# Optimization experiments

Hardware: AMD Instinct MI355X
Metric: run time of the kernel (lower is better)

## Reference

```python
import jax, jax.numpy as jnp
import numpy as np

DIM = 2048; N_HEADS = 16; Q_RANK = 1536; KV_RANK = 192
NOPE = 128; ROPE = 64; QK_HD = NOPE + ROPE  # 192 == KV_RANK (required by k_norm/cache widths)
B = 2; S = 2048; MAX_SEQ = 2048
EPS = 1e-6
SCALE = QK_HD ** -0.5


def _rms(v, w):
    return v * jax.lax.rsqrt(jnp.mean(v * v, axis=-1, keepdims=True) + EPS) * w


def _rope(v, cos, sin):
    # v: [..., d] with interleaved (even, odd) pairs, cos/sin broadcastable to [..., d//2]
    vr = v.reshape(v.shape[:-1] + (-1, 2))
    a, b = vr[..., 0], vr[..., 1]
    return jnp.stack([a * cos - b * sin, a * sin + b * cos], axis=-1).reshape(v.shape)


def setup_inputs() -> dict:
    key = jax.random.key(0)
    ks = jax.random.split(key, 8)
    std = 0.02
    x = jax.random.normal(ks[0], (B, S, DIM), jnp.float32)
    # rotary tables: [S, ROPE//2, 2] = (cos, sin)
    t = jnp.arange(S, dtype=jnp.float32)
    inv = 1.0 / (10000.0 ** (jnp.arange(0, ROPE, 2, dtype=jnp.float32) / ROPE))
    ang = jnp.outer(t, inv)
    freqs_cis = jnp.stack([jnp.cos(ang), jnp.sin(ang)], axis=-1)
    mask = jnp.triu(jnp.full((S, S), -1e9, jnp.float32), k=1)  # causal additive mask
    c_kv_cache = jnp.zeros((B, MAX_SEQ, KV_RANK), jnp.float32)
    return {
        "x": x, "start_pos": 0, "freqs_cis": freqs_cis, "mask": mask,
        "c_kv_cache": c_kv_cache,
        "wqa_w": jax.random.normal(ks[1], (Q_RANK, DIM), jnp.float32) * std,
        "wqa_b": jnp.zeros((Q_RANK,), jnp.float32),
        "wqb_w": jax.random.normal(ks[2], (N_HEADS * QK_HD, Q_RANK), jnp.float32) * std,
        "wqb_b": jnp.zeros((N_HEADS * QK_HD,), jnp.float32),
        "q_norm_w": jnp.ones((Q_RANK,), jnp.float32),
        "wkva_w": jax.random.normal(ks[3], (QK_HD, DIM), jnp.float32) * std,
        "wkva_b": jnp.zeros((QK_HD,), jnp.float32),
        "k_norm_w": jnp.ones((KV_RANK,), jnp.float32),
        "wuk_w": jax.random.normal(ks[4], (NOPE, NOPE), jnp.float32) * std,
        "wuk_b": jnp.zeros((NOPE,), jnp.float32),
        "wuv_w": jax.random.normal(ks[5], (DIM, NOPE), jnp.float32) * std,
        "wuv_b": jnp.zeros((DIM,), jnp.float32),
    }


def reference(x, start_pos, freqs_cis, mask, c_kv_cache,
              wqa_w, wqa_b, wqb_w, wqb_b, q_norm_w,
              wkva_w, wkva_b, k_norm_w, wuk_w, wuk_b, wuv_w, wuv_b):
    bsz, seqlen, _ = x.shape
    end = start_pos + seqlen
    cos, sin = freqs_cis[..., 0], freqs_cis[..., 1]  # [seqlen, ROPE//2]

    # low-rank Q path: down-proj -> RMSNorm -> up-proj -> per-head split
    q = _rms(x @ wqa_w.T + wqa_b, q_norm_w)
    q = (q @ wqb_w.T + wqb_b).reshape(bsz, seqlen, N_HEADS, QK_HD)
    q_nope, q_pe = q[..., :NOPE], q[..., NOPE:]
    q_pe = _rope(q_pe, cos[None, :, None, :], sin[None, :, None, :])

    # latent KV path: project -> RMSNorm -> partial RoPE -> scatter into cache
    kv = _rms(x @ wkva_w.T + wkva_b, k_norm_w)  # [b, s, KV_RANK]
    k_pe = _rope(kv[..., NOPE:], cos[None, :, :], sin[None, :, :])
    kv = jnp.concatenate([kv[..., :NOPE], k_pe], axis=-1)
    cache = jax.lax.dynamic_update_slice(c_kv_cache, kv, (0, start_pos, 0))
    keys = cache[:bsz, :end]  # [b, t, KV_RANK]
    k_nope, k_rope = keys[..., :NOPE], keys[..., NOPE:]

    # absorbed attention: fold w_uk into the query side, attend in latent space
    q_abs = q_nope @ wuk_w.T + wuk_b  # [b, s, h, NOPE]
    scores = (jnp.einsum('bshd,btd->bsht', q_abs, k_nope)
              + jnp.einsum('bshr,btr->bsht', q_pe, k_rope)) * SCALE
    scores = scores + mask[None, :seqlen, None, :end]
    attn = jax.nn.softmax(scores, axis=-1)
    out = jnp.einsum('bsht,btd->bshd', attn, k_nope)  # latent values
    out = (out @ wuv_w.T + wuv_b).sum(axis=2)  # up-project values, merge heads -> [b, s, dim]
    return out
```

## Files before the change

kernel.cpp:

```cpp
#include <hip/hip_runtime.h>
#include <hip/hip_bf16.h>
#include <stdint.h>

#define NH     16
#define QRANK  1536
#define NOPE_  128
#define QKHD   192
#define B_     2
#define S_     2048
#define MAXSEQ 2048
#define EPS_   1e-6f
#define SCALE_ 0.07216878364870322f

typedef __attribute__((ext_vector_type(4))) float f32x4;
typedef __attribute__((ext_vector_type(8))) short short8;
typedef __attribute__((ext_vector_type(4))) short short4v;

__device__ inline short f2bf(float f){
  uint32_t u = __builtin_bit_cast(uint32_t, f);
  uint32_t r = (u + 0x7FFFu + ((u >> 16) & 1u)) >> 16;
  return (short)(uint16_t)r;
}
__device__ inline float bf2f(short s){
  uint32_t u = ((uint32_t)(uint16_t)s) << 16;
  return __builtin_bit_cast(float, u);
}

__global__ void k_f2b(const float* __restrict__ in, short* __restrict__ out, long n){
  long i = ((long)blockIdx.x * blockDim.x + threadIdx.x) * 4;
  long stride = (long)gridDim.x * blockDim.x * 4;
  for(; i < n; i += stride){
    float4 v = *reinterpret_cast<const float4*>(in + i);
    short4v o;
    o.x = f2bf(v.x); o.y = f2bf(v.y); o.z = f2bf(v.z); o.w = f2bf(v.w);
    *reinterpret_cast<short4v*>(out + i) = o;
  }
}

template<int BN, bool OUT_BF16>
__global__ __launch_bounds__(256)
void k_gemm_bt(const short* __restrict__ A, const short* __restrict__ Bm,
               const float* __restrict__ bias, float biasScale,
               void* __restrict__ Cp, int M, int N, int K, int ldc)
{
  constexpr int BM = 128, PAD = 40;
  constexpr int WN = BN / 2, FN = WN / 16;
  __shared__ short As[BM * PAD];
  __shared__ short Bs[BN * PAD];
  const int tid = threadIdx.x;
  const int l = tid & 63, wid = tid >> 6;
  const int wr = wid >> 1, wc = wid & 1;
  const long m0 = (long)blockIdx.x * BM;
  const long n0 = (long)blockIdx.y * BN;
  const int lrow = l & 15, lk = (l >> 4) * 8;

  f32x4 acc[4][FN];
  for(int m = 0; m < 4; m++) for(int n = 0; n < FN; n++) acc[m][n] = (f32x4)0.0f;

  for(int kt = 0; kt < K; kt += 32){
    #pragma unroll
    for(int i = 0; i < BM/64; i++){
      int c = tid + 256*i;
      int row = c >> 2, ko = (c & 3) * 8;
      short8 v = *reinterpret_cast<const short8*>(&A[(m0 + row)*(long)K + kt + ko]);
      *reinterpret_cast<short8*>(&As[row*PAD + ko]) = v;
    }
    #pragma unroll
    for(int i = 0; i < BN/64; i++){
      int c = tid + 256*i;
      int row = c >> 2, ko = (c & 3) * 8;
      short8 v = *reinterpret_cast<const short8*>(&Bm[(n0 + row)*(long)K + kt + ko]);
      *reinterpret_cast<short8*>(&Bs[row*PAD + ko]) = v;
    }
    __syncthreads();
    short8 af[4], bfv[FN];
    #pragma unroll
    for(int m = 0; m < 4; m++)
      af[m] = *reinterpret_cast<const short8*>(&As[(wr*64 + m*16 + lrow)*PAD + lk]);
    #pragma unroll
    for(int n = 0; n < FN; n++)
      bfv[n] = *reinterpret_cast<const short8*>(&Bs[(wc*WN + n*16 + lrow)*PAD + lk]);
    #pragma unroll
    for(int m = 0; m < 4; m++)
      #pragma unroll
      for(int n = 0; n < FN; n++)
        acc[m][n] = __builtin_amdgcn_mfma_f32_16x16x32_bf16(af[m], bfv[n], acc[m][n], 0, 0, 0);
    __syncthreads();
  }
  #pragma unroll
  for(int m = 0; m < 4; m++){
    int row_l = wr*64 + m*16 + (l >> 4)*4;
    #pragma unroll
    for(int n = 0; n < FN; n++){
      int col = (int)n0 + wc*WN + n*16 + (l & 15);
      float bv = bias ? bias[col]*biasScale : 0.0f;
      #pragma unroll
      for(int r = 0; r < 4; r++){
        long row = m0 + row_l + r;
        float v = acc[m][n][r] + bv;
        if constexpr (OUT_BF16) ((short*)Cp)[row*(long)ldc + col] = f2bf(v);
        else                    ((float*)Cp)[row*(long)ldc + col] = v;
      }
    }
  }
}

__global__ __launch_bounds__(256)
void k_rms_q(const float* __restrict__ in, const float* __restrict__ w,
             short* __restrict__ out)
{
  const int row = blockIdx.x;
  const int tid = threadIdx.x;
  const float* p = in + (long)row * QRANK;
  float v[6]; float ss = 0.0f;
  #pragma unroll
  for(int i = 0; i < 6; i++){ v[i] = p[tid + 256*i]; ss += v[i]*v[i]; }
  #pragma unroll
  for(int off = 1; off < 64; off <<= 1) ss += __shfl_xor(ss, off);
  __shared__ float red[4];
  if((tid & 63) == 0) red[tid >> 6] = ss;
  __syncthreads();
  ss = red[0] + red[1] + red[2] + red[3];
  float scale = rsqrtf(ss / (float)QRANK + EPS_);
  #pragma unroll
  for(int i = 0; i < 6; i++){
    int c = tid + 256*i;
    out[(long)row*QRANK + c] = f2bf(v[i] * scale * w[c]);
  }
}

__global__ __launch_bounds__(256)
void k_qassemble(const short* __restrict__ q, const float* __restrict__ freqs,
                 short* __restrict__ qn, short* __restrict__ qfull)
{
  int wid = threadIdx.x >> 6, l = threadIdx.x & 63;
  long hr = (long)blockIdx.x*4 + wid;
  long bs = hr >> 4; int h = (int)(hr & 15);
  int s = (int)(bs & (S_ - 1));
  const short* src = q + bs*3072 + h*QKHD;
  qn[hr*128 + l]      = src[l];
  qn[hr*128 + 64 + l] = src[64 + l];
  float v = bf2f(src[128 + l]);
  int i = l >> 1;
  float cs = freqs[(s*32 + i)*2], sn = freqs[(s*32 + i)*2 + 1];
  float pv = __shfl_xor(v, 1);
  float r = (l & 1) ? (pv*sn + v*cs) : (v*cs - pv*sn);
  qfull[hr*QKHD + 128 + l] = f2bf(r);
}

__global__ __launch_bounds__(256)
void k_kvproc(const float* __restrict__ kvf, const float* __restrict__ w,
              const float* __restrict__ freqs, const float* __restrict__ cache,
              const int* __restrict__ sp_ptr, short* __restrict__ kf)
{
  int wid = threadIdx.x >> 6, l = threadIdx.x & 63;
  long row = (long)blockIdx.x*4 + wid;
  int b = (int)(row >> 11);
  int t = (int)(row & (MAXSEQ - 1));
  int sp = sp_ptr[0];
  int end = sp + S_;
  if(t < sp){
    const float* c = cache + row*QKHD;
    kf[row*QKHD + l]       = f2bf(c[l]);
    kf[row*QKHD + 64 + l]  = f2bf(c[64 + l]);
    kf[row*QKHD + 128 + l] = f2bf(c[128 + l]);
    return;
  }
  if(t >= end) return;
  int s = t - sp;
  const float* p = kvf + ((long)b*S_ + s)*QKHD;
  float v0 = p[l], v1 = p[64 + l], v2 = p[128 + l];
  float ss = v0*v0 + v1*v1 + v2*v2;
  #pragma unroll
  for(int off = 1; off < 64; off <<= 1) ss += __shfl_xor(ss, off);
  float scale = rsqrtf(ss / (float)QKHD + EPS_);
  float n0 = v0*scale*w[l], n1 = v1*scale*w[64 + l], n2 = v2*scale*w[128 + l];
  kf[row*QKHD + l]      = f2bf(n0);
  kf[row*QKHD + 64 + l] = f2bf(n1);
  int i = l >> 1;
  float cs = freqs[(s*32 + i)*2], sn = freqs[(s*32 + i)*2 + 1];
  float pv = __shfl_xor(n2, 1);
  float r = (l & 1) ? (pv*sn + n2*cs) : (n2*cs - pv*sn);
  kf[row*QKHD + 128 + l] = f2bf(r);
}

__global__ __launch_bounds__(256)
void k_vtrans(const short* __restrict__ kf, short* __restrict__ vt)
{
  __shared__ short T[32 * 132];
  const int b = blockIdx.y;
  const int t0 = blockIdx.x * 32;
  const int tid = threadIdx.x;
  #pragma unroll
  for(int i = 0; i < 4; i++){
    int c = tid + 256*i;
    int tr = c >> 5, dg = c & 31;
    short4v v = *reinterpret_cast<const short4v*>(&kf[((long)b*MAXSEQ + t0 + tr)*QKHD + dg*4]);
    *reinterpret_cast<short4v*>(&T[tr*132 + dg*4]) = v;
  }
  __syncthreads();
  #pragma unroll
  for(int i = 0; i < 4; i++){
    int c = tid + 256*i;
    int dr = c >> 3, tg = c & 7;
    short4v v;
    v.x = T[(tg*4 + 0)*132 + dr];
    v.y = T[(tg*4 + 1)*132 + dr];
    v.z = T[(tg*4 + 2)*132 + dr];
    v.w = T[(tg*4 + 3)*132 + dr];
    *reinterpret_cast<short4v*>(&vt[((long)b*128 + dr)*MAXSEQ + t0 + tg*4]) = v;
  }
}

__global__ __launch_bounds__(256, 3)
void k_attn3(const short* __restrict__ qfull, const short* __restrict__ kf,
             const short* __restrict__ vt, const int* __restrict__ sp_ptr,
             short* __restrict__ oh)
{
  __shared__ short Ks[64 * 192];
  __shared__ short Vs[128 * 64];
  __shared__ short Ps[4][16 * 68];
  const int tid = threadIdx.x;
  const int l = tid & 63, w = tid >> 6;
  const int lrow = l & 15, lhi = l >> 4;
  const int h = blockIdx.y, b = blockIdx.z;
  const int sp = sp_ptr[0];
  const long kbase = (long)b * MAXSEQ;
  const long vbase = (long)b * 128;

  short8 kreg[6], vreg[4];

  #pragma unroll 1
  for(int part = 0; part < 2; part++){
    const int tile = part ? (31 - (int)blockIdx.x) : (int)blockIdx.x;
    const int q0 = tile * 64;

    short8 qa[6];
    {
      int s = q0 + w*16 + lrow;
      const short* qp = qfull + (((long)b*S_ + s)*NH + h)*QKHD + lhi*8;
      #pragma unroll
      for(int ks = 0; ks < 6; ks++) qa[ks] = *reinterpret_cast<const short8*>(qp + ks*32);
    }
    f32x4 o[8];
    #pragma unroll
    for(int df = 0; df < 8; df++) o[df] = (f32x4)0.0f;
    float mrun[4], lrun[4];
    #pragma unroll
    for(int i = 0; i < 4; i++){ mrun[i] = -1e30f; lrun[i] = 0.0f; }

    int hi = q0 + 64 + sp;
    int nt = (hi + 63) >> 6; if(nt > (MAXSEQ >> 6)) nt = MAXSEQ >> 6;

    {
      const int T0 = 0;
      #pragma unroll
      for(int i = 0; i < 6; i++){
        int cid = tid + 256*i;  int r = cid/24, c = cid%24;
        kreg[i] = *reinterpret_cast<const short8*>(&kf[(kbase + T0 + r)*QKHD + c*8]);
      }
      #pragma unroll
      for(int i = 0; i < 4; i++){
        int cid = tid + 256*i;  int r = cid >> 3, c = cid & 7;
        vreg[i] = *reinterpret_cast<const short8*>(&vt[(vbase + r)*MAXSEQ + T0 + c*8]);
      }
      #pragma unroll
      for(int i = 0; i < 6; i++){
        int cid = tid + 256*i;  int r = cid/24, c = cid%24;
        *reinterpret_cast<short8*>(&Ks[r*192 + (c ^ (r & 7))*8]) = kreg[i];
      }
      #pragma unroll
      for(int i = 0; i < 4; i++){
        int cid = tid + 256*i;  int r = cid >> 3, c = cid & 7;
        *reinterpret_cast<short8*>(&Vs[r*64 + (c ^ (r & 7))*8]) = vreg[i];
      }
    }
    __syncthreads();

    for(int t0 = 0; t0 < nt; t0++){
      const int T0 = t0 * 64;
      if(t0 + 1 < nt){
        const int Tn = T0 + 64;
        #pragma unroll
        for(int i = 0; i < 6; i++){
          int cid = tid + 256*i;  int r = cid/24, c = cid%24;
          kreg[i] = *reinterpret_cast<const short8*>(&kf[(kbase + Tn + r)*QKHD + c*8]);
        }
        #pragma unroll
        for(int i = 0; i < 4; i++){
          int cid = tid + 256*i;  int r = cid >> 3, c = cid & 7;
          vreg[i] = *reinterpret_cast<const short8*>(&vt[(vbase + r)*MAXSEQ + Tn + c*8]);
        }
      }
      f32x4 sc[4];
      #pragma unroll
      for(int tf = 0; tf < 4; tf++) sc[tf] = (f32x4)0.0f;
      #pragma unroll
      for(int ks = 0; ks < 6; ks++){
        #pragma unroll
        for(int tf = 0; tf < 4; tf++){
          int krow = tf*16 + lrow;
          int cs = (ks*4 + lhi) ^ (lrow & 7);
          short8 bfr = *reinterpret_cast<const short8*>(&Ks[krow*192 + cs*8]);
          sc[tf] = __builtin_amdgcn_mfma_f32_16x16x32_bf16(qa[ks], bfr, sc[tf], 0, 0, 0);
        }
      }
      const bool needmask = (T0 + 63 > q0 + w*16 + sp);
      #pragma unroll
      for(int rr = 0; rr < 4; rr++){
        int q = q0 + w*16 + lhi*4 + rr;
        float s0 = sc[0][rr]*SCALE_, s1 = sc[1][rr]*SCALE_;
        float s2 = sc[2][rr]*SCALE_, s3 = sc[3][rr]*SCALE_;
        if(needmask){
          int t = T0 + lrow;
          if(t      > q + sp) s0 = -1e30f;
          if(t + 16 > q + sp) s1 = -1e30f;
          if(t + 32 > q + sp) s2 = -1e30f;
          if(t + 48 > q + sp) s3 = -1e30f;
        }
        float mx = fmaxf(fmaxf(s0, s1), fmaxf(s2, s3));
        #pragma unroll
        for(int off = 1; off < 16; off <<= 1) mx = fmaxf(mx, __shfl_xor(mx, off));
        float mnew = fmaxf(mrun[rr], mx);
        float corr = __expf(mrun[rr] - mnew);
        float p0 = __expf(s0 - mnew), p1 = __expf(s1 - mnew);
        float p2 = __expf(s2 - mnew), p3 = __expf(s3 - mnew);
        float psum = (p0 + p1) + (p2 + p3);
        #pragma unroll
        for(int off = 1; off < 16; off <<= 1) psum += __shfl_xor(psum, off);
        lrun[rr] = lrun[rr]*corr + psum;
        mrun[rr] = mnew;
        #pragma unroll
        for(int df = 0; df < 8; df++) o[df][rr] *= corr;
        int prow = lhi*4 + rr;
        Ps[w][prow*68 + lrow]      = f2bf(p0);
        Ps[w][prow*68 + 16 + lrow] = f2bf(p1);
        Ps[w][prow*68 + 32 + lrow] = f2bf(p2);
        Ps[w][prow*68 + 48 + lrow] = f2bf(p3);
      }
      short8 pa[2];
      #pragma unroll
      for(int kc = 0; kc < 2; kc++)
        pa[kc] = *reinterpret_cast<const short8*>(&Ps[w][lrow*68 + kc*32 + lhi*8]);
      #pragma unroll
      for(int df = 0; df < 8; df++){
        #pragma unroll
        for(int kc = 0; kc < 2; kc++){
          int vrow = df*16 + lrow;
          int cs = (kc*4 + lhi) ^ (lrow & 7);
          short8 vfr = *reinterpret_cast<const short8*>(&Vs[vrow*64 + cs*8]);
          o[df] = __builtin_amdgcn_mfma_f32_16x16x32_bf16(pa[kc], vfr, o[df], 0, 0, 0);
        }
      }
      __syncthreads();
      if(t0 + 1 < nt){
        #pragma unroll
        for(int i = 0; i < 6; i++){
          int cid = tid + 256*i;  int r = cid/24, c = cid%24;
          *reinterpret_cast<short8*>(&Ks[r*192 + (c ^ (r & 7))*8]) = kreg[i];
        }
        #pragma unroll
        for(int i = 0; i < 4; i++){
          int cid = tid + 256*i;  int r = cid >> 3, c = cid & 7;
          *reinterpret_cast<short8*>(&Vs[r*64 + (c ^ (r & 7))*8]) = vreg[i];
        }
        __syncthreads();
      }
    }
    #pragma unroll
    for(int rr = 0; rr < 4; rr++){
      int s = q0 + w*16 + lhi*4 + rr;
      float inv = 1.0f / lrun[rr];
      #pragma unroll
      for(int df = 0; df < 8; df++)
        oh[(((long)b*S_ + s)*NH + h)*128 + df*16 + lrow] = f2bf(o[df][rr] * inv);
    }
  }
}

__global__ void k_redheads(const short* __restrict__ ohp, short* __restrict__ hs){
  long row = blockIdx.x;
  int d = threadIdx.x;
  float acc = 0.0f;
  #pragma unroll
  for(int h = 0; h < NH; h++) acc += bf2f(ohp[(row*NH + h)*128 + d]);
  hs[row*128 + d] = f2bf(acc);
}

static constexpr size_t OFF_X16   = 0;
static constexpr size_t OFF_WQA   = 16777216;
static constexpr size_t OFF_WQB   = 23068672;
static constexpr size_t OFF_WKV   = 32505856;
static constexpr size_t OFF_WUK   = 33292288;
static constexpr size_t OFF_WUV   = 33325056;
static constexpr size_t OFF_QNORM = 33849344;
static constexpr size_t OFF_QFULL = 46432256;
static constexpr size_t OFF_KFULL = 71598080;
static constexpr size_t OFF_HSUM  = 73170944;
static constexpr size_t OFF_SCR   = 74219520;
static constexpr size_t OFF_QA    = OFF_SCR;
static constexpr size_t OFF_Q16   = OFF_SCR;
static constexpr size_t OFF_QN    = OFF_SCR + 25165824;
static constexpr size_t OFF_KVF   = OFF_SCR + 41943040;
static constexpr size_t OFF_OH    = OFF_SCR;
static constexpr size_t OFF_VT    = OFF_SCR + 25165824;

extern "C" void kernel_launch(void* const* d_in, const int* in_sizes, int n_in,
                              void* d_out, int out_size, void* d_ws, size_t ws_size,
                              hipStream_t stream)
{
  const float* x      = (const float*)d_in[0];
  const int*   sp     = (const int*)  d_in[1];
  const float* freqs  = (const float*)d_in[2];
  const float* cache  = (const float*)d_in[4];
  const float* wqa_w  = (const float*)d_in[5];
  const float* wqa_b  = (const float*)d_in[6];
  const float* wqb_w  = (const float*)d_in[7];
  const float* wqb_b  = (const float*)d_in[8];
  const float* qnw    = (const float*)d_in[9];
  const float* wkva_w = (const float*)d_in[10];
  const float* wkva_b = (const float*)d_in[11];
  const float* knw    = (const float*)d_in[12];
  const float* wuk_w  = (const float*)d_in[13];
  const float* wuk_b  = (const float*)d_in[14];
  const float* wuv_w  = (const float*)d_in[15];
  const float* wuv_b  = (const float*)d_in[16];

  char* ws = (char*)d_ws;
  short* X16   = (short*)(ws + OFF_X16);
  short* WQA16 = (short*)(ws + OFF_WQA);
  short* WQB16 = (short*)(ws + OFF_WQB);
  short* WKV16 = (short*)(ws + OFF_WKV);
  short* WUK16 = (short*)(ws + OFF_WUK);
  short* WUV16 = (short*)(ws + OFF_WUV);
  short* QNORM = (short*)(ws + OFF_QNORM);
  short* QFULL = (short*)(ws + OFF_QFULL);
  short* KFULL = (short*)(ws + OFF_KFULL);
  short* HSUM  = (short*)(ws + OFF_HSUM);
  float* QA    = (float*)(ws + OFF_QA);
  short* Q16   = (short*)(ws + OFF_Q16);
  short* QN16  = (short*)(ws + OFF_QN);
  float* KVF   = (float*)(ws + OFF_KVF);
  short* OH16  = (short*)(ws + OFF_OH);
  short* VT16  = (short*)(ws + OFF_VT);

  auto cvt = [&](const float* src, short* dst, long n){
    long blocks = (n/4 + 255) / 256; if(blocks > 2048) blocks = 2048;
    k_f2b<<<(int)blocks, 256, 0, stream>>>(src, dst, n);
  };
  cvt(x,      X16,   (long)B_*S_*2048);
  cvt(wqa_w,  WQA16, (long)QRANK*2048);
  cvt(wqb_w,  WQB16, (long)NH*QKHD*QRANK);
  cvt(wkva_w, WKV16, (long)QKHD*2048);
  cvt(wuk_w,  WUK16, (long)NOPE_*NOPE_);
  cvt(wuv_w,  WUV16, (long)2048*NOPE_);

  k_gemm_bt<128,false><<<dim3(32,12), 256, 0, stream>>>(X16, WQA16, wqa_b, 1.0f, QA, 4096, QRANK, 2048, QRANK);
  k_rms_q<<<4096, 256, 0, stream>>>(QA, qnw, QNORM);
  k_gemm_bt<128,true><<<dim3(32,24), 256, 0, stream>>>(QNORM, WQB16, wqb_b, 1.0f, Q16, 4096, NH*QKHD, QRANK, NH*QKHD);
  k_qassemble<<<16384, 256, 0, stream>>>(Q16, freqs, QN16, QFULL);
  k_gemm_bt<128,true><<<dim3(512,1), 256, 0, stream>>>(QN16, WUK16, wuk_b, 1.0f, QFULL, 65536, 128, 128, QKHD);
  k_gemm_bt<64,false><<<dim3(32,3), 256, 0, stream>>>(X16, WKV16, wkva_b, 1.0f, KVF, 4096, QKHD, 2048, QKHD);
  k_kvproc<<<1024, 256, 0, stream>>>(KVF, knw, freqs, cache, sp, KFULL);
  k_vtrans<<<dim3(64,2), 256, 0, stream>>>(KFULL, VT16);
  k_attn3<<<dim3(16,16,2), 256, 0, stream>>>(QFULL, KFULL, VT16, sp, OH16);
  k_redheads<<<4096, 128, 0, stream>>>(OH16, HSUM);
  k_gemm_bt<128,false><<<dim3(32,16), 256, 0, stream>>>(HSUM, WUV16, wuv_b, 16.0f, (float*)d_out, 4096, 2048, NOPE_, 2048);
}
```

Baseline: 524.6 us.

## Add direct global-to-LDS GEMM and split attention into one tile per block

Adds a new GEMM kernel that stages 128x32 bf16 tiles straight into LDS with global_load_lds instead of going through registers, and uses it for four of the projection GEMMs. The attention kernel no longer pairs two query tiles per block for causal load balance: it launches 32 blocks per head, each handling one tile, with the largest tiles scheduled first. The GEMM drops register staging but has no double buffering and no LDS padding or swizzle, so bank conflicts and exposed load latency are possible. The attention change gives the scheduler more blocks in exchange for uneven per-block work.

```diff
diff --git a/kernel.cpp b/kernel.cpp
--- a/kernel.cpp
+++ b/kernel.cpp
@@ -25,6 +25,10 @@
   uint32_t u = ((uint32_t)(uint16_t)s) << 16;
   return __builtin_bit_cast(float, u);
 }
+__device__ inline void gload16(const short* g, short* l){
+  __builtin_amdgcn_global_load_lds((const __attribute__((address_space(1))) void*)g,
+                                   (__attribute__((address_space(3))) void*)l, 16, 0, 0);
+}
 
 __global__ void k_f2b(const float* __restrict__ in, short* __restrict__ out, long n){
   long i = ((long)blockIdx.x * blockDim.x + threadIdx.x) * 4;
@@ -34,6 +38,77 @@
     short4v o;
     o.x = f2bf(v.x); o.y = f2bf(v.y); o.z = f2bf(v.z); o.w = f2bf(v.w);
     *reinterpret_cast<short4v*>(out + i) = o;
+  }
+}
+
+template<bool OUT_BF16>
+__global__ __launch_bounds__(256)
+void k_gemm97(const short* __restrict__ A, const short* __restrict__ Bm,
+              const float* __restrict__ bias, float biasScale,
+              void* __restrict__ Cp, int M, int N, int K, int ldc)
+{
+  __shared__ short As[128 * 32];
+  __shared__ short Bs[128 * 32];
+  const int tid = threadIdx.x;
+  const int l = tid & 63, w = tid >> 6;
+  const int wr = w >> 1, wc = w & 1;
+  const long m0 = (long)blockIdx.x * 128;
+  const long n0 = (long)blockIdx.y * 128;
+  const int lrow = l & 15, lk8 = (l >> 4) * 8;
+
+  int ci0 = (w*2 + 0)*64 + l, ci1 = (w*2 + 1)*64 + l;
+  const int r0 = ci0 >> 2, c0 = (ci0 & 3) * 8;
+  const int r1 = ci1 >> 2, c1 = (ci1 & 3) * 8;
+  const short* a0 = &A[(m0 + r0)*(long)K + c0];
+  const short* a1 = &A[(m0 + r1)*(long)K + c1];
+  const short* b0 = &Bm[(n0 + r0)*(long)K + c0];
+  const short* b1 = &Bm[(n0 + r1)*(long)K + c1];
+  short* lA0 = &As[(w*2 + 0)*512];
+  short* lA1 = &As[(w*2 + 1)*512];
+  short* lB0 = &Bs[(w*2 + 0)*512];
+  short* lB1 = &Bs[(w*2 + 1)*512];
+
+  f32x4 acc[4][4];
+  #pragma unroll
+  for(int m = 0; m < 4; m++)
+    #pragma unroll
+    for(int n = 0; n < 4; n++) acc[m][n] = (f32x4)0.0f;
+
+  for(int kt = 0; kt < K; kt += 32){
+    gload16(a0 + kt, lA0);
+    gload16(a1 + kt, lA1);
+    gload16(b0 + kt, lB0);
+    gload16(b1 + kt, lB1);
+    __syncthreads();
+    short8 af[4], bfv[4];
+    #pragma unroll
+    for(int m = 0; m < 4; m++)
+      af[m] = *reinterpret_cast<const short8*>(&As[(wr*64 + m*16 + lrow)*32 + lk8]);
+    #pragma unroll
+    for(int n = 0; n < 4; n++)
+      bfv[n] = *reinterpret_cast<const short8*>(&Bs[(wc*64 + n*16 + lrow)*32 + lk8]);
+    #pragma unroll
+    for(int m = 0; m < 4; m++)
+      #pragma unroll
+      for(int n = 0; n < 4; n++)
+        acc[m][n] = __builtin_amdgcn_mfma_f32_16x16x32_bf16(af[m], bfv[n], acc[m][n], 0, 0, 0);
+    __syncthreads();
+  }
+  #pragma unroll
+  for(int m = 0; m < 4; m++){
+    int row_l = wr*64 + m*16 + (l >> 4)*4;
+    #pragma unroll
+    for(int n = 0; n < 4; n++){
+      int col = (int)n0 + wc*64 + n*16 + lrow;
+      float bv = bias ? bias[col]*biasScale : 0.0f;
+      #pragma unroll
+      for(int r = 0; r < 4; r++){
+        long row = m0 + row_l + r;
+        float v = acc[m][n][r] + bv;
+        if constexpr (OUT_BF16) ((short*)Cp)[row*(long)ldc + col] = f2bf(v);
+        else                    ((float*)Cp)[row*(long)ldc + col] = v;
+      }
+    }
   }
 }
 
@@ -213,7 +288,7 @@
 }
 
 __global__ __launch_bounds__(256, 3)
-void k_attn3(const short* __restrict__ qfull, const short* __restrict__ kf,
+void k_attn4(const short* __restrict__ qfull, const short* __restrict__ kf,
              const short* __restrict__ vt, const int* __restrict__ sp_ptr,
              short* __restrict__ oh)
 {
@@ -229,41 +304,127 @@
   const long vbase = (long)b * 128;
 
   short8 kreg[6], vreg[4];
-
-  #pragma unroll 1
-  for(int part = 0; part < 2; part++){
-    const int tile = part ? (31 - (int)blockIdx.x) : (int)blockIdx.x;
-    const int q0 = tile * 64;
-
-    short8 qa[6];
-    {
-      int s = q0 + w*16 + lrow;
-      const short* qp = qfull + (((long)b*S_ + s)*NH + h)*QKHD + lhi*8;
-      #pragma unroll
-      for(int ks = 0; ks < 6; ks++) qa[ks] = *reinterpret_cast<const short8*>(qp + ks*32);
-    }
-    f32x4 o[8];
-    #pragma unroll
-    for(int df = 0; df < 8; df++) o[df] = (f32x4)0.0f;
-    float mrun[4], lrun[4];
-    #pragma unroll
-    for(int i = 0; i < 4; i++){ mrun[i] = -1e30f; lrun[i] = 0.0f; }
-
-    int hi = q0 + 64 + sp;
-    int nt = (hi + 63) >> 6; if(nt > (MAXSEQ >> 6)) nt = MAXSEQ >> 6;
-
-    {
-      const int T0 = 0;
+  const int tile = 31 - (int)blockIdx.x;
+  const int q0 = tile * 64;
+
+  short8 qa[6];
+  {
+    int s = q0 + w*16 + lrow;
+    const short* qp = qfull + (((long)b*S_ + s)*NH + h)*QKHD + lhi*8;
+    #pragma unroll
+    for(int ks = 0; ks < 6; ks++) qa[ks] = *reinterpret_cast<const short8*>(qp + ks*32);
+  }
+  f32x4 o[8];
+  #pragma unroll
+  for(int df = 0; df < 8; df++) o[df] = (f32x4)0.0f;
+  float mrun[4], lrun[4];
+  #pragma unroll
+  for(int i = 0; i < 4; i++){ mrun[i] = -1e30f; lrun[i] = 0.0f; }
+
+  int hi = q0 + 64 + sp;
+  int nt = (hi + 63) >> 6; if(nt > (MAXSEQ >> 6)) nt = MAXSEQ >> 6;
+
+  {
+    #pragma unroll
+    for(int i = 0; i < 6; i++){
+      int cid = tid + 256*i;  int r = cid/24, c = cid%24;
+      kreg[i] = *reinterpret_cast<const short8*>(&kf[(kbase + r)*QKHD + c*8]);
+    }
+    #pragma unroll
+    for(int i = 0; i < 4; i++){
+      int cid = tid + 256*i;  int r = cid >> 3, c = cid & 7;
+      vreg[i] = *reinterpret_cast<const short8*>(&vt[(vbase + r)*MAXSEQ + c*8]);
+    }
+    #pragma unroll
+    for(int i = 0; i < 6; i++){
+      int cid = tid + 256*i;  int r = cid/24, c = cid%24;
+      *reinterpret_cast<short8*>(&Ks[r*192 + (c ^ (r & 7))*8]) = kreg[i];
+    }
+    #pragma unroll
+    for(int i = 0; i < 4; i++){
+      int cid = tid + 256*i;  int r = cid >> 3, c = cid & 7;
+      *reinterpret_cast<short8*>(&Vs[r*64 + (c ^ (r & 7))*8]) = vreg[i];
+    }
+  }
+  __syncthreads();
+
+  for(int t0 = 0; t0 < nt; t0++){
+    const int T0 = t0 * 64;
+    if(t0 + 1 < nt){
+      const int Tn = T0 + 64;
       #pragma unroll
       for(int i = 0; i < 6; i++){
         int cid = tid + 256*i;  int r = cid/24, c = cid%24;
-        kreg[i] = *reinterpret_cast<const short8*>(&kf[(kbase + T0 + r)*QKHD + c*8]);
+        kreg[i] = *reinterpret_cast<const short8*>(&kf[(kbase + Tn + r)*QKHD + c*8]);
       }
       #pragma unroll
       for(int i = 0; i < 4; i++){
         int cid = tid + 256*i;  int r = cid >> 3, c = cid & 7;
-        vreg[i] = *reinterpret_cast<const short8*>(&vt[(vbase + r)*MAXSEQ + T0 + c*8]);
-      }
+        vreg[i] = *reinterpret_cast<const short8*>(&vt[(vbase + r)*MAXSEQ + Tn + c*8]);
+      }
+    }
+    f32x4 sc[4];
+    #pragma unroll
+    for(int tf = 0; tf < 4; tf++) sc[tf] = (f32x4)0.0f;
+    #pragma unroll
+    for(int ks = 0; ks < 6; ks++){
+      #pragma unroll
+      for(int tf = 0; tf < 4; tf++){
+        int krow = tf*16 + lrow;
+        int cs = (ks*4 + lhi) ^ (lrow & 7);
+        short8 bfr = *reinterpret_cast<const short8*>(&Ks[krow*192 + cs*8]);
+        sc[tf] = __builtin_amdgcn_mfma_f32_16x16x32_bf16(qa[ks], bfr, sc[tf], 0, 0, 0);
+      }
+    }
+    const bool needmask = (T0 + 63 > q0 + w*16 + sp);
+    #pragma unroll
+    for(int rr = 0; rr < 4; rr++){
+      int q = q0 + w*16 + lhi*4 + rr;
+      float s0 = sc[0][rr]*SCALE_, s1 = sc[1][rr]*SCALE_;
+      float s2 = sc[2][rr]*SCALE_, s3 = sc[3][rr]*SCALE_;
+      if(needmask){
+        int t = T0 + lrow;
+        if(t      > q + sp) s0 = -1e30f;
+        if(t + 16 > q + sp) s1 = -1e30f;
+        if(t + 32 > q + sp) s2 = -1e30f;
+        if(t + 48 > q + sp) s3 = -1e30f;
+      }
+      float mx = fmaxf(fmaxf(s0, s1), fmaxf(s2, s3));
+      #pragma unroll
+      for(int off = 1; off < 16; off <<= 1) mx = fmaxf(mx, __shfl_xor(mx, off));
+      float mnew = fmaxf(mrun[rr], mx);
+      float corr = __expf(mrun[rr] - mnew);
+      float p0 = __expf(s0 - mnew), p1 = __expf(s1 - mnew);
+      float p2 = __expf(s2 - mnew), p3 = __expf(s3 - mnew);
+      float psum = (p0 + p1) + (p2 + p3);
+      #pragma unroll
+      for(int off = 1; off < 16; off <<= 1) psum += __shfl_xor(psum, off);
+      lrun[rr] = lrun[rr]*corr + psum;
+      mrun[rr] = mnew;
+      #pragma unroll
+      for(int df = 0; df < 8; df++) o[df][rr] *= corr;
+      int prow = lhi*4 + rr;
+      Ps[w][prow*68 + lrow]      = f2bf(p0);
+      Ps[w][prow*68 + 16 + lrow] = f2bf(p1);
+      Ps[w][prow*68 + 32 + lrow] = f2bf(p2);
+      Ps[w][prow*68 + 48 + lrow] = f2bf(p3);
+    }
+    short8 pa[2];
+    #pragma unroll
+    for(int kc = 0; kc < 2; kc++)
+      pa[kc] = *reinterpret_cast<const short8*>(&Ps[w][lrow*68 + kc*32 + lhi*8]);
+    #pragma unroll
+    for(int df = 0; df < 8; df++){
+      #pragma unroll
+      for(int kc = 0; kc < 2; kc++){
+        int vrow = df*16 + lrow;
+        int cs = (kc*4 + lhi) ^ (lrow & 7);
+        short8 vfr = *reinterpret_cast<const short8*>(&Vs[vrow*64 + cs*8]);
+        o[df] = __builtin_amdgcn_mfma_f32_16x16x32_bf16(pa[kc], vfr, o[df], 0, 0, 0);
+      }
+    }
+    __syncthreads();
+    if(t0 + 1 < nt){
       #pragma unroll
       for(int i = 0; i < 6; i++){
         int cid = tid + 256*i;  int r = cid/24, c = cid%24;
@@ -274,107 +435,16 @@
         int cid = tid + 256*i;  int r = cid >> 3, c = cid & 7;
         *reinterpret_cast<short8*>(&Vs[r*64 + (c ^ (r & 7))*8]) = vreg[i];
       }
-    }
-    __syncthreads();
-
-    for(int t0 = 0; t0 < nt; t0++){
-      const int T0 = t0 * 64;
-      if(t0 + 1 < nt){
-        const int Tn = T0 + 64;
-        #pragma unroll
-        for(int i = 0; i < 6; i++){
-          int cid = tid + 256*i;  int r = cid/24, c = cid%24;
-          kreg[i] = *reinterpret_cast<const short8*>(&kf[(kbase + Tn + r)*QKHD + c*8]);
-        }
-        #pragma unroll
-        for(int i = 0; i < 4; i++){
-          int cid = tid + 256*i;  int r = cid >> 3, c = cid & 7;
-          vreg[i] = *reinterpret_cast<const short8*>(&vt[(vbase + r)*MAXSEQ + Tn + c*8]);
-        }
-      }
-      f32x4 sc[4];
-      #pragma unroll
-      for(int tf = 0; tf < 4; tf++) sc[tf] = (f32x4)0.0f;
-      #pragma unroll
-      for(int ks = 0; ks < 6; ks++){
-        #pragma unroll
-        for(int tf = 0; tf < 4; tf++){
-          int krow = tf*16 + lrow;
-          int cs = (ks*4 + lhi) ^ (lrow & 7);
-          short8 bfr = *reinterpret_cast<const short8*>(&Ks[krow*192 + cs*8]);
-          sc[tf] = __builtin_amdgcn_mfma_f32_16x16x32_bf16(qa[ks], bfr, sc[tf], 0, 0, 0);
-        }
-      }
-      const bool needmask = (T0 + 63 > q0 + w*16 + sp);
-      #pragma unroll
-      for(int rr = 0; rr < 4; rr++){
-        int q = q0 + w*16 + lhi*4 + rr;
-        float s0 = sc[0][rr]*SCALE_, s1 = sc[1][rr]*SCALE_;
-        float s2 = sc[2][rr]*SCALE_, s3 = sc[3][rr]*SCALE_;
-        if(needmask){
-          int t = T0 + lrow;
-          if(t      > q + sp) s0 = -1e30f;
-          if(t + 16 > q + sp) s1 = -1e30f;
-          if(t + 32 > q + sp) s2 = -1e30f;
-          if(t + 48 > q + sp) s3 = -1e30f;
-        }
-        float mx = fmaxf(fmaxf(s0, s1), fmaxf(s2, s3));
-        #pragma unroll
-        for(int off = 1; off < 16; off <<= 1) mx = fmaxf(mx, __shfl_xor(mx, off));
-        float mnew = fmaxf(mrun[rr], mx);
-        float corr = __expf(mrun[rr] - mnew);
-        float p0 = __expf(s0 - mnew), p1 = __expf(s1 - mnew);
-        float p2 = __expf(s2 - mnew), p3 = __expf(s3 - mnew);
-        float psum = (p0 + p1) + (p2 + p3);
-        #pragma unroll
-        for(int off = 1; off < 16; off <<= 1) psum += __shfl_xor(psum, off);
-        lrun[rr] = lrun[rr]*corr + psum;
-        mrun[rr] = mnew;
-        #pragma unroll
-        for(int df = 0; df < 8; df++) o[df][rr] *= corr;
-        int prow = lhi*4 + rr;
-        Ps[w][prow*68 + lrow]      = f2bf(p0);
-        Ps[w][prow*68 + 16 + lrow] = f2bf(p1);
-        Ps[w][prow*68 + 32 + lrow] = f2bf(p2);
-        Ps[w][prow*68 + 48 + lrow] = f2bf(p3);
-      }
-      short8 pa[2];
-      #pragma unroll
-      for(int kc = 0; kc < 2; kc++)
-        pa[kc] = *reinterpret_cast<const short8*>(&Ps[w][lrow*68 + kc*32 + lhi*8]);
-      #pragma unroll
-      for(int df = 0; df < 8; df++){
-        #pragma unroll
-        for(int kc = 0; kc < 2; kc++){
-          int vrow = df*16 + lrow;
-          int cs = (kc*4 + lhi) ^ (lrow & 7);
-          short8 vfr = *reinterpret_cast<const short8*>(&Vs[vrow*64 + cs*8]);
-          o[df] = __builtin_amdgcn_mfma_f32_16x16x32_bf16(pa[kc], vfr, o[df], 0, 0, 0);
-        }
-      }
       __syncthreads();
-      if(t0 + 1 < nt){
-        #pragma unroll
-        for(int i = 0; i < 6; i++){
-          int cid = tid + 256*i;  int r = cid/24, c = cid%24;
-          *reinterpret_cast<short8*>(&Ks[r*192 + (c ^ (r & 7))*8]) = kreg[i];
-        }
-        #pragma unroll
-        for(int i = 0; i < 4; i++){
-          int cid = tid + 256*i;  int r = cid >> 3, c = cid & 7;
-          *reinterpret_cast<short8*>(&Vs[r*64 + (c ^ (r & 7))*8]) = vreg[i];
-        }
-        __syncthreads();
-      }
-    }
-    #pragma unroll
-    for(int rr = 0; rr < 4; rr++){
-      int s = q0 + w*16 + lhi*4 + rr;
-      float inv = 1.0f / lrun[rr];
-      #pragma unroll
-      for(int df = 0; df < 8; df++)
-        oh[(((long)b*S_ + s)*NH + h)*128 + df*16 + lrow] = f2bf(o[df][rr] * inv);
-    }
+    }
+  }
+  #pragma unroll
+  for(int rr = 0; rr < 4; rr++){
+    int s = q0 + w*16 + lhi*4 + rr;
+    float inv = 1.0f / lrun[rr];
+    #pragma unroll
+    for(int df = 0; df < 8; df++)
+      oh[(((long)b*S_ + s)*NH + h)*128 + df*16 + lrow] = f2bf(o[df][rr] * inv);
   }
 }
 
@@ -455,15 +525,15 @@
   cvt(wuk_w,  WUK16, (long)NOPE_*NOPE_);
   cvt(wuv_w,  WUV16, (long)2048*NOPE_);
 
-  k_gemm_bt<128,false><<<dim3(32,12), 256, 0, stream>>>(X16, WQA16, wqa_b, 1.0f, QA, 4096, QRANK, 2048, QRANK);
+  k_gemm97<false><<<dim3(32,12), 256, 0, stream>>>(X16, WQA16, wqa_b, 1.0f, QA, 4096, QRANK, 2048, QRANK);
   k_rms_q<<<4096, 256, 0, stream>>>(QA, qnw, QNORM);
-  k_gemm_bt<128,true><<<dim3(32,24), 256, 0, stream>>>(QNORM, WQB16, wqb_b, 1.0f, Q16, 4096, NH*QKHD, QRANK, NH*QKHD);
+  k_gemm97<true><<<dim3(32,24), 256, 0, stream>>>(QNORM, WQB16, wqb_b, 1.0f, Q16, 4096, NH*QKHD, QRANK, NH*QKHD);
   k_qassemble<<<16384, 256, 0, stream>>>(Q16, freqs, QN16, QFULL);
-  k_gemm_bt<128,true><<<dim3(512,1), 256, 0, stream>>>(QN16, WUK16, wuk_b, 1.0f, QFULL, 65536, 128, 128, QKHD);
+  k_gemm97<true><<<dim3(512,1), 256, 0, stream>>>(QN16, WUK16, wuk_b, 1.0f, QFULL, 65536, 128, 128, QKHD);
   k_gemm_bt<64,false><<<dim3(32,3), 256, 0, stream>>>(X16, WKV16, wkva_b, 1.0f, KVF, 4096, QKHD, 2048, QKHD);
   k_kvproc<<<1024, 256, 0, stream>>>(KVF, knw, freqs, cache, sp, KFULL);
   k_vtrans<<<dim3(64,2), 256, 0, stream>>>(KFULL, VT16);
-  k_attn3<<<dim3(16,16,2), 256, 0, stream>>>(QFULL, KFULL, VT16, sp, OH16);
+  k_attn4<<<dim3(32,16,2), 256, 0, stream>>>(QFULL, KFULL, VT16, sp, OH16);
   k_redheads<<<4096, 128, 0, stream>>>(OH16, HSUM);
-  k_gemm_bt<128,false><<<dim3(32,16), 256, 0, stream>>>(HSUM, WUV16, wuv_b, 16.0f, (float*)d_out, 4096, 2048, NOPE_, 2048);
-}
+  k_gemm97<false><<<dim3(32,16), 256, 0, stream>>>(HSUM, WUV16, wuv_b, 16.0f, (float*)d_out, 4096, 2048, NOPE_, 2048);
+}
```

Result: slower. 654.0 us (+24.7%).
